# Performance work log

Measured on AMD Instinct MI355X. Metric: run time of the kernel, lower is better.

Reference implementation:

```python
import jax, jax.numpy as jnp
import numpy as np

# ---- static config ----
SCALES = [1, 2, 3, 4, 6, 9, 13, 19, 27, 40, 60, 88, 128]
L = sum(SCALES)            # 400
FIRST_L = SCALES[0]        # 1
C = 1024                   # emb_dim (C == D)
DEPTH = 8
H = 16
DH = C // H
CVAE = 64
V = 4096
ND = 256                   # node_embed_size
MLP = 4 * C
B = 32
EPS = 1e-6

_LVL = np.concatenate([np.full(pn, i, dtype=np.int32) for i, pn in enumerate(SCALES)])  # [L]
_BIAS = np.where(_LVL[:, None] >= _LVL[None, :], 0.0, -np.inf).astype(np.float32)        # [L,L]


def _ln(x):
    # LayerNorm without affine params (VAR's ln_wo_grad), eps=1e-6
    m = jnp.mean(x, axis=-1, keepdims=True)
    v = jnp.mean(jnp.square(x - m), axis=-1, keepdims=True)
    return (x - m) * jax.lax.rsqrt(v + EPS)


def setup_inputs() -> dict:
    key = jax.random.key(0)
    ks = iter(jax.random.split(key, 40))
    def p(shape, s=0.02):
        return jax.random.normal(next(ks), shape, dtype=jnp.float32) * s
    inp = {
        "x_BLCv_wo_first_l": jax.random.normal(next(ks), (B, L - FIRST_L, CVAE), jnp.float32),
        "poc_context": jax.random.normal(next(ks), (B, L, CVAE), jnp.float32),
        "poc_cond": jax.random.normal(next(ks), (B, ND), jnp.float32),
        # embedders / positional
        "word_w": p((CVAE, C)), "word_b": p((C,)),
        "poc_w": p((ND, C)), "poc_b": p((C,)),
        "pos_start": p((1, FIRST_L, C)),
        "pos_1LC": p((1, L, C)),
        "lvl_tab": p((len(SCALES), C)),
        # shared AdaLN (SiLU -> Linear(D, 6C))
        "ada_w": p((C, 6 * C)), "ada_b": p((6 * C,)),
        # per-block params, stacked over depth
        "ada_gss": p((DEPTH, 1, 1, 6, C)),
        "q_w": p((DEPTH, C, C)), "q_b": p((DEPTH, C)),
        "kv_w": p((DEPTH, C, 2 * C)), "kv_b": p((DEPTH, 2 * C)),
        "proj_w": p((DEPTH, C, C)), "proj_b": p((DEPTH, C)),
        "fc1_w": p((DEPTH, C, MLP)), "fc1_b": p((DEPTH, MLP)),
        "fc2_w": p((DEPTH, MLP, C)), "fc2_b": p((DEPTH, C)),
        # AdaLNBeforeHead (SiLU -> Linear(D, 2C)) + head
        "head_ada_w": p((C, 2 * C)), "head_ada_b": p((2 * C,)),
        "head_w": p((C, V)), "head_b": p((V,)),
    }
    return inp


def reference(x_BLCv_wo_first_l, poc_context, poc_cond,
              word_w, word_b, poc_w, poc_b, pos_start, pos_1LC, lvl_tab,
              ada_w, ada_b, ada_gss, q_w, q_b, kv_w, kv_b, proj_w, proj_b,
              fc1_w, fc1_b, fc2_w, fc2_b, head_ada_w, head_ada_b, head_w, head_b):
    lvl_idx = jnp.asarray(_LVL)
    bias = jnp.asarray(_BIAS)                      # [L,L] block scale-causal
    scale = 1.0 / np.sqrt(DH)

    cond = poc_cond @ poc_w + poc_b                # [B,C] (cond_BD == sos source)
    sos = cond[:, None, :] + pos_start             # [B,first_l,C]
    x = jnp.concatenate([sos, x_BLCv_wo_first_l @ word_w + word_b], axis=1)  # [B,L,C]
    lvl = lvl_tab[lvl_idx] + pos_1LC[0]            # [L,C]
    x = x + lvl
    poc = (poc_context @ word_w + word_b) + lvl    # [B,L,C]

    gss = jax.nn.silu(cond) @ ada_w + ada_b        # [B,6C]
    gss = gss.reshape(B, 1, 6, C)

    def block(x, params):
        ag, qw, qb, kvw, kvb, pw, pb, f1w, f1b, f2w, f2b = params
        mod = ag + gss                             # [B,1,6,C]
        g1, g2, s1, s2, sh1, sh2 = [mod[:, :, i] for i in range(6)]  # each [B,1,C]
        # cross-attention (q from modulated x, kv from poc context), scale-causal bias
        xn = _ln(x) * (1.0 + s1) + sh1
        q = (xn @ qw + qb).reshape(B, L, H, DH)
        kv = (poc @ kvw + kvb).reshape(B, L, 2, H, DH)
        k, v = kv[:, :, 0], kv[:, :, 1]
        att = jnp.einsum('bqhd,bkhd->bhqk', q, k) * scale + bias
        att = jax.nn.softmax(att, axis=-1)
        o = jnp.einsum('bhqk,bkhd->bqhd', att, v).reshape(B, L, C)
        x = x + g1 * (o @ pw + pb)
        # FFN with AdaLN modulation
        xn2 = _ln(x) * (1.0 + s2) + sh2
        hdn = jax.nn.gelu(xn2 @ f1w + f1b, approximate=False)
        x = x + g2 * (hdn @ f2w + f2b)
        return x, None

    x, _ = jax.lax.scan(block, x, (ada_gss, q_w, q_b, kv_w, kv_b, proj_w, proj_b,
                                   fc1_w, fc1_b, fc2_w, fc2_b))

    # AdaLNBeforeHead + head
    ss = jax.nn.silu(cond) @ head_ada_w + head_ada_b   # [B,2C]
    h_scale, h_shift = ss[:, None, :C], ss[:, None, C:]
    x = _ln(x) * (1.0 + h_scale) + h_shift
    logits = x @ head_w + head_b                       # [B,L,V]
    return logits
```

## Files before the change

kernel.cpp:

```cpp
#include <hip/hip_runtime.h>
#include <hip/hip_bf16.h>
#include <math.h>

#define DEV __device__ __forceinline__

typedef __attribute__((ext_vector_type(4))) float f32x4;
typedef __attribute__((ext_vector_type(8))) short bf16x8;
typedef __attribute__((ext_vector_type(4))) short s16x4;

static constexpr int Bz = 32, Lz = 400, Cz = 1024, MLPz = 4096;
static constexpr int BL = Bz * Lz;

DEV float bf2f(unsigned short u) {
  union { unsigned int i; float f; } v; v.i = ((unsigned int)u) << 16; return v.f;
}
DEV unsigned short f2bf(float f) {
  union { float f; unsigned int i; } v; v.f = f;
  unsigned int r = v.i + 0x7FFFu + ((v.i >> 16) & 1u);
  return (unsigned short)(r >> 16);
}

DEV int level_of(int l) {
  const int cum[13] = {1,3,6,10,16,25,38,57,84,124,184,272,400};
  int lv = 12;
  #pragma unroll
  for (int i = 12; i >= 0; i--) if (l < cum[i]) lv = i;
  return lv;
}
DEV int row_kmax(int l) {
  const int cum[13] = {1,3,6,10,16,25,38,57,84,124,184,272,400};
  int km = 400;
  #pragma unroll
  for (int i = 12; i >= 0; i--) if (l < cum[i]) km = cum[i];
  return km;
}

DEV void stage16(const unsigned short* g, unsigned short* l) {
#if __has_builtin(__builtin_amdgcn_global_load_lds)
  __builtin_amdgcn_global_load_lds((const __attribute__((address_space(1))) void*)g,
                                   (__attribute__((address_space(3))) void*)l, 16, 0, 0);
#else
  *(bf16x8*)l = *(const bf16x8*)g;
#endif
}

__global__ __launch_bounds__(256)
void tconv_k(const float* __restrict__ in, unsigned short* __restrict__ out, int K, int N)
{
  __shared__ float t[64][65];
  const int n0 = blockIdx.x * 64, k0 = blockIdx.y * 64;
  #pragma unroll
  for (int i = 0; i < 16; i++) {
    int idx = i * 256 + threadIdx.x;
    int r = idx >> 6, c = idx & 63;
    t[r][c] = in[(size_t)(k0 + r) * N + n0 + c];
  }
  __syncthreads();
  #pragma unroll
  for (int i = 0; i < 16; i++) {
    int idx = i * 256 + threadIdx.x;
    int rn = idx >> 6, ck = idx & 63;
    out[(size_t)(n0 + rn) * K + k0 + ck] = f2bf(t[ck][rn]);
  }
}

__global__ __launch_bounds__(256)
void tconv5_k(const float* __restrict__ qw, const float* __restrict__ kvw,
              const float* __restrict__ pjw, const float* __restrict__ f1w,
              unsigned short* __restrict__ qwt, unsigned short* __restrict__ kvwt,
              unsigned short* __restrict__ pjwt, unsigned short* __restrict__ f1wt)
{
  const int bid = blockIdx.x;
  const float* in; unsigned short* out; int N, n0, k0;
  if (bid < 256)       { in = qw;  out = qwt;  N = 1024; int t = bid;        n0 = (t & 15) * 64; k0 = (t >> 4) * 64; }
  else if (bid < 768)  { in = kvw; out = kvwt; N = 2048; int t = bid - 256;  n0 = (t & 31) * 64; k0 = (t >> 5) * 64; }
  else if (bid < 1024) { in = pjw; out = pjwt; N = 1024; int t = bid - 768;  n0 = (t & 15) * 64; k0 = (t >> 4) * 64; }
  else                 { in = f1w; out = f1wt; N = 4096; int t = bid - 1024; n0 = (t & 63) * 64; k0 = (t >> 6) * 64; }
  __shared__ float tt[64][65];
  #pragma unroll
  for (int i = 0; i < 16; i++) {
    int idx = i * 256 + threadIdx.x;
    int r = idx >> 6, c = idx & 63;
    tt[r][c] = in[(size_t)(k0 + r) * N + n0 + c];
  }
  __syncthreads();
  #pragma unroll
  for (int i = 0; i < 16; i++) {
    int idx = i * 256 + threadIdx.x;
    int rn = idx >> 6, ck = idx & 63;
    out[(size_t)(n0 + rn) * 1024 + k0 + ck] = f2bf(tt[ck][rn]);
  }
}

enum { EP_BF16 = 0, EP_GELU = 1, EP_RESID = 2, EP_F32 = 3, EP_KV = 4 };

template<int MODE>
__global__ __launch_bounds__(256, 2)
void gemm2_k(const unsigned short* __restrict__ A, const unsigned short* __restrict__ Bt,
             const float* __restrict__ bias, void* __restrict__ out,
             float* __restrict__ xres, const float* __restrict__ gsh,
             const float* __restrict__ gpb, unsigned short* __restrict__ vtb,
             int N, int K)
{
  __shared__ unsigned short As[128 * 64];
  __shared__ unsigned short Bs[128 * 64];
  const int tid = threadIdx.x;
  const int lane = tid & 63, wv = tid >> 6;
  const int row0 = blockIdx.x * 128, col0 = blockIdx.y * 128;
  const int wm = (wv >> 1) * 64, wn = (wv & 1) * 64;

  f32x4 acc[4][4] = {};

  for (int k0 = 0; k0 < K; k0 += 64) {
    #pragma unroll
    for (int i = 0; i < 4; i++) {
      int ch = i * 256 + tid;
      int r = ch >> 3;
      int c8 = (ch & 7) ^ (r & 7);
      stage16(A + (size_t)(row0 + r) * K + k0 + c8 * 8, As + ch * 8);
    }
    #pragma unroll
    for (int i = 0; i < 4; i++) {
      int ch = i * 256 + tid;
      int r = ch >> 3;
      int c8 = (ch & 7) ^ (r & 7);
      stage16(Bt + (size_t)(col0 + r) * K + k0 + c8 * 8, Bs + ch * 8);
    }
    __syncthreads();
    #pragma unroll
    for (int kk = 0; kk < 2; kk++) {
      bf16x8 af[4], bfr[4];
      const int bcol = kk * 64 + (lane >> 4) * 16;
      #pragma unroll
      for (int m = 0; m < 4; m++) {
        int r = wm + m * 16 + (lane & 15);
        af[m] = *(const bf16x8*)((char*)As + r * 128 + (bcol ^ ((r & 7) << 4)));
      }
      #pragma unroll
      for (int n = 0; n < 4; n++) {
        int r = wn + n * 16 + (lane & 15);
        bfr[n] = *(const bf16x8*)((char*)Bs + r * 128 + (bcol ^ ((r & 7) << 4)));
      }
      #pragma unroll
      for (int m = 0; m < 4; m++)
        #pragma unroll
        for (int n = 0; n < 4; n++)
          acc[m][n] = __builtin_amdgcn_mfma_f32_16x16x32_bf16(af[m], bfr[n], acc[m][n], 0, 0, 0);
    }
    __syncthreads();
  }

  const int rbase = row0 + wm + ((lane >> 4) << 2);
  const int cbase = col0 + wn + (lane & 15);
  #pragma unroll
  for (int n = 0; n < 4; n++) {
    int gcol = cbase + n * 16;
    float bv = bias[gcol];
    #pragma unroll
    for (int m = 0; m < 4; m++) {
      #pragma unroll
      for (int r = 0; r < 4; r++) {
        int grow = rbase + m * 16 + r;
        float v = acc[m][n][r] + bv;
        if constexpr (MODE == EP_BF16) {
          ((unsigned short*)out)[(size_t)grow * N + gcol] = f2bf(v);
        } else if constexpr (MODE == EP_GELU) {
          float g = 0.5f * v * (1.f + erff(v * 0.70710678118654752f));
          ((unsigned short*)out)[(size_t)grow * N + gcol] = f2bf(g);
        } else if constexpr (MODE == EP_RESID) {
          int b = grow / Lz;
          float g = gsh[gcol] + gpb[(size_t)b * 6144 + gcol];
          xres[(size_t)grow * Cz + gcol] += g * v;
        } else if constexpr (MODE == EP_KV) {
          if (gcol < 1024) {
            ((unsigned short*)out)[(size_t)grow * 1024 + gcol] = f2bf(v);
          } else {
            int b = grow / Lz, l = grow - b * Lz;
            int h = (gcol >> 6) & 15, d = gcol & 63;
            vtb[(((size_t)b * 16 + h) * 64 + d) * Lz + l] = f2bf(v);
          }
        } else {
          ((float*)out)[(size_t)grow * N + gcol] = v;
        }
      }
    }
  }
}

__global__ __launch_bounds__(256, 2)
void qkv_k(const unsigned short* __restrict__ xn, const unsigned short* __restrict__ poc,
           const unsigned short* __restrict__ qwt, const unsigned short* __restrict__ kvwt,
           const float* __restrict__ q_bias, const float* __restrict__ kv_bias,
           unsigned short* __restrict__ qbf, unsigned short* __restrict__ kbuf,
           unsigned short* __restrict__ vtb)
{
  __shared__ unsigned short As[128 * 64];
  __shared__ unsigned short Bs[128 * 64];
  const int tid = threadIdx.x;
  const int lane = tid & 63, wv = tid >> 6;
  const bool isq = blockIdx.y < 8;
  const unsigned short* A  = isq ? xn : poc;
  const unsigned short* Bt = isq ? qwt : kvwt;
  const float* bias        = isq ? q_bias : kv_bias;
  const int K = 1024;
  const int row0 = blockIdx.x * 128;
  const int col0 = (isq ? blockIdx.y : (blockIdx.y - 8)) * 128;
  const int wm = (wv >> 1) * 64, wn = (wv & 1) * 64;

  f32x4 acc[4][4] = {};

  for (int k0 = 0; k0 < K; k0 += 64) {
    #pragma unroll
    for (int i = 0; i < 4; i++) {
      int ch = i * 256 + tid;
      int r = ch >> 3;
      int c8 = (ch & 7) ^ (r & 7);
      stage16(A + (size_t)(row0 + r) * K + k0 + c8 * 8, As + ch * 8);
    }
    #pragma unroll
    for (int i = 0; i < 4; i++) {
      int ch = i * 256 + tid;
      int r = ch >> 3;
      int c8 = (ch & 7) ^ (r & 7);
      stage16(Bt + (size_t)(col0 + r) * K + k0 + c8 * 8, Bs + ch * 8);
    }
    __syncthreads();
    #pragma unroll
    for (int kk = 0; kk < 2; kk++) {
      bf16x8 af[4], bfr[4];
      const int bcol = kk * 64 + (lane >> 4) * 16;
      #pragma unroll
      for (int m = 0; m < 4; m++) {
        int r = wm + m * 16 + (lane & 15);
        af[m] = *(const bf16x8*)((char*)As + r * 128 + (bcol ^ ((r & 7) << 4)));
      }
      #pragma unroll
      for (int n = 0; n < 4; n++) {
        int r = wn + n * 16 + (lane & 15);
        bfr[n] = *(const bf16x8*)((char*)Bs + r * 128 + (bcol ^ ((r & 7) << 4)));
      }
      #pragma unroll
      for (int m = 0; m < 4; m++)
        #pragma unroll
        for (int n = 0; n < 4; n++)
          acc[m][n] = __builtin_amdgcn_mfma_f32_16x16x32_bf16(af[m], bfr[n], acc[m][n], 0, 0, 0);
    }
    __syncthreads();
  }

  const int rbase = row0 + wm + ((lane >> 4) << 2);
  const int cbase = col0 + wn + (lane & 15);
  #pragma unroll
  for (int n = 0; n < 4; n++) {
    int gcol = cbase + n * 16;
    float bv = bias[gcol];
    #pragma unroll
    for (int m = 0; m < 4; m++) {
      #pragma unroll
      for (int r = 0; r < 4; r++) {
        int grow = rbase + m * 16 + r;
        float v = acc[m][n][r] + bv;
        if (isq) {
          qbf[(size_t)grow * 1024 + gcol] = f2bf(v);
        } else if (gcol < 1024) {
          kbuf[(size_t)grow * 1024 + gcol] = f2bf(v);
        } else {
          int b = grow / Lz, l = grow - b * Lz;
          int h = (gcol >> 6) & 15, d = gcol & 63;
          vtb[(((size_t)b * 16 + h) * 64 + d) * Lz + l] = f2bf(v);
        }
      }
    }
  }
}

__global__ __launch_bounds__(256)
void ln2_k(const float* __restrict__ x, unsigned short* __restrict__ out,
           const float* __restrict__ ssh, const float* __restrict__ spb, int sstride,
           const float* __restrict__ hsh, const float* __restrict__ hpb, int hstride)
{
  const int wv = threadIdx.x >> 6, lane = threadIdx.x & 63;
  const int row = blockIdx.x * 4 + wv;
  const int b = row / Lz;
  const float* xr = x + (size_t)row * Cz;
  f32x4 v[4];
  float s1 = 0.f;
  #pragma unroll
  for (int j = 0; j < 4; j++) {
    v[j] = *(const f32x4*)(xr + j * 256 + lane * 4);
    s1 += v[j][0] + v[j][1] + v[j][2] + v[j][3];
  }
  #pragma unroll
  for (int o = 32; o > 0; o >>= 1) s1 += __shfl_xor(s1, o, 64);
  float mean = s1 * (1.f / 1024.f);
  float s2 = 0.f;
  #pragma unroll
  for (int j = 0; j < 4; j++)
    #pragma unroll
    for (int i = 0; i < 4; i++) { float d = v[j][i] - mean; s2 += d * d; }
  #pragma unroll
  for (int o = 32; o > 0; o >>= 1) s2 += __shfl_xor(s2, o, 64);
  float rstd = rsqrtf(s2 * (1.f / 1024.f) + 1e-6f);
  #pragma unroll
  for (int j = 0; j < 4; j++) {
    s16x4 o4;
    #pragma unroll
    for (int i = 0; i < 4; i++) {
      int c = j * 256 + lane * 4 + i;
      float sc = (ssh ? ssh[c] : 0.f) + spb[(size_t)b * sstride + c];
      float sh = (hsh ? hsh[c] : 0.f) + hpb[(size_t)b * hstride + c];
      o4[i] = (short)f2bf((v[j][i] - mean) * rstd * (1.f + sc) + sh);
    }
    *(s16x4*)(&out[(size_t)row * Cz + j * 256 + lane * 4]) = o4;
  }
}

__global__ __launch_bounds__(512)
void attn3_k(const unsigned short* __restrict__ qb,
             const unsigned short* __restrict__ kbuf,
             const unsigned short* __restrict__ vtb,
             unsigned short* __restrict__ ob)
{
  __shared__ unsigned short Ks[400 * 64];
  __shared__ unsigned short Vt[64 * 408];
  __shared__ unsigned short Pl[8][512];
  const int bh = blockIdx.x, b = bh >> 4, h = bh & 15;
  const int qc = blockIdx.y;
  const int tid = threadIdx.x;
  const int q0 = qc * 128;
  const int nch = (row_kmax(min(q0 + 127, Lz - 1)) + 15) >> 4;

  const size_t kbase = (size_t)b * Lz * 1024 + h * 64;
  for (int i = tid; i < nch * 128; i += 512) {
    int l = i >> 3, d8 = i & 7;
    bf16x8 kr = *(const bf16x8*)&kbuf[kbase + (size_t)l * 1024 + d8 * 8];
    *(bf16x8*)((char*)Ks + l * 128 + ((d8 * 16) ^ ((l & 7) << 4))) = kr;
  }
  const size_t vbase = ((size_t)b * 16 + h) * 64 * Lz;
  const int vch = nch * 2;
  for (int i = tid; i < 3200; i += 512) {
    int d = i / 50, c8 = i - d * 50;
    if (c8 < vch)
      *(bf16x8*)((char*)Vt + d * 816 + c8 * 16) = *(const bf16x8*)&vtb[vbase + (size_t)d * Lz + c8 * 8];
  }
  __syncthreads();

  const int wv = tid >> 6, lane = tid & 63, g = lane >> 4, q = lane & 15;
  const int qw0 = q0 + wv * 16;
  if (qw0 >= Lz) return;
  const int qrow = qw0 + q;
  const int my_kmax = row_kmax(qrow);
  const int nsch = (row_kmax(qw0 + 15) + 31) >> 5;
  const int vclamp = nch * 16 - 8;

  const unsigned short* qp = qb + (size_t)(b * Lz + qrow) * Cz + h * 64;
  bf16x8 qf0 = *(const bf16x8*)(qp + g * 8);
  bf16x8 qf1 = *(const bf16x8*)(qp + 32 + g * 8);
  unsigned short* myP = &Pl[wv][0];

  float m = -30000.f, lsum = 0.f;
  f32x4 acc[4] = {};

  for (int sc = 0; sc < nsch; ++sc) {
    f32x4 st0 = {0.f,0.f,0.f,0.f}, st1 = {0.f,0.f,0.f,0.f};
    {
      int kr = sc * 32 + q;
      const char* kb = (const char*)Ks + kr * 128;
      int sw = (kr & 7) << 4;
      bf16x8 k0 = *(const bf16x8*)(kb + ((g * 16) ^ sw));
      bf16x8 k1 = *(const bf16x8*)(kb + ((64 + g * 16) ^ sw));
      st0 = __builtin_amdgcn_mfma_f32_16x16x32_bf16(k0, qf0, st0, 0, 0, 0);
      st0 = __builtin_amdgcn_mfma_f32_16x16x32_bf16(k1, qf1, st0, 0, 0, 0);
    }
    {
      int kr = sc * 32 + 16 + q;
      const char* kb = (const char*)Ks + kr * 128;
      int sw = (kr & 7) << 4;
      bf16x8 k0 = *(const bf16x8*)(kb + ((g * 16) ^ sw));
      bf16x8 k1 = *(const bf16x8*)(kb + ((64 + g * 16) ^ sw));
      st1 = __builtin_amdgcn_mfma_f32_16x16x32_bf16(k0, qf0, st1, 0, 0, 0);
      st1 = __builtin_amdgcn_mfma_f32_16x16x32_bf16(k1, qf1, st1, 0, 0, 0);
    }

    float s8[8]; float cmax = -30000.f;
    #pragma unroll
    for (int r = 0; r < 4; r++) {
      int k0g = sc * 32 + 4 * g + r;
      int k1g = k0g + 16;
      s8[r]     = (k0g < my_kmax) ? st0[r] * 0.125f : -30000.f;
      s8[4 + r] = (k1g < my_kmax) ? st1[r] * 0.125f : -30000.f;
      cmax = fmaxf(cmax, fmaxf(s8[r], s8[4 + r]));
    }
    cmax = fmaxf(cmax, __shfl_xor(cmax, 16, 64));
    cmax = fmaxf(cmax, __shfl_xor(cmax, 32, 64));

    if (!__all(cmax <= m + 8.f)) {
      float mnew = fmaxf(m, cmax);
      float f = __expf(m - mnew);
      lsum *= f;
      #pragma unroll
      for (int blk = 0; blk < 4; blk++)
        #pragma unroll
        for (int j = 0; j < 4; j++) acc[blk][j] *= f;
      m = mnew;
    }

    float p[8], ps = 0.f;
    #pragma unroll
    for (int r = 0; r < 8; r++) { p[r] = __expf(s8[r] - m); ps += p[r]; }
    ps += __shfl_xor(ps, 16, 64);
    ps += __shfl_xor(ps, 32, 64);
    lsum += ps;

    #pragma unroll
    for (int cp = 0; cp < 2; cp++) {
      #pragma unroll
      for (int j = 0; j < 2; j++) {
        unsigned int pk;
        asm("v_cvt_pk_bf16_f32 %0, %1, %2" : "=v"(pk)
            : "v"(p[4 * cp + 2 * j]), "v"(p[4 * cp + 2 * j + 1]));
        int w = 8 * cp + 2 * g + j;
        *(unsigned int*)((char*)myP + q * 64 + 4 * (w ^ q)) = pk;
      }
    }

    unsigned int pw[4];
    #pragma unroll
    for (int i = 0; i < 4; i++)
      pw[i] = *(const unsigned int*)((const char*)myP + q * 64 + 4 * ((4 * g + i) ^ q));
    bf16x8 pfrag;
    #pragma unroll
    for (int i = 0; i < 4; i++) {
      pfrag[2 * i]     = (short)(pw[i] & 0xFFFF);
      pfrag[2 * i + 1] = (short)(pw[i] >> 16);
    }

    const int koff = min(sc * 32 + 8 * g, vclamp);
    #pragma unroll
    for (int blk = 0; blk < 4; blk++) {
      bf16x8 vf = *(const bf16x8*)((const char*)Vt + (16 * blk + q) * 816 + koff * 2);
      acc[blk] = __builtin_amdgcn_mfma_f32_16x16x32_bf16(vf, pfrag, acc[blk], 0, 0, 0);
    }
  }

  float inv = 1.f / lsum;
  unsigned short* op = ob + (size_t)(b * Lz + qrow) * Cz + h * 64;
  #pragma unroll
  for (int blk = 0; blk < 4; blk++)
    #pragma unroll
    for (int r = 0; r < 4; r++)
      op[16 * blk + 4 * g + r] = f2bf(acc[blk][r] * inv);
}

__global__ __launch_bounds__(256)
void cond_k(const float* __restrict__ pc, const float* __restrict__ pw,
            const float* __restrict__ pb, float* __restrict__ cond,
            float* __restrict__ silu)
{
  const int b = blockIdx.y;
  const int n = blockIdx.x * 256 + threadIdx.x;
  __shared__ float a[256];
  a[threadIdx.x] = pc[b * 256 + threadIdx.x];
  __syncthreads();
  float s = pb[n];
  for (int k = 0; k < 256; k++) s += a[k] * pw[(size_t)k * Cz + n];
  cond[(size_t)b * Cz + n] = s;
  silu[(size_t)b * Cz + n] = s / (1.f + __expf(-s));
}

__global__ __launch_bounds__(256)
void smallmm_k(const float* __restrict__ A, const float* __restrict__ W,
               const float* __restrict__ bias, float* __restrict__ out, int N)
{
  const int b = blockIdx.y;
  const int n = blockIdx.x * 256 + threadIdx.x;
  __shared__ float a[1024];
  for (int i = threadIdx.x; i < 1024; i += 256) a[i] = A[(size_t)b * 1024 + i];
  __syncthreads();
  float s = bias[n];
  for (int k = 0; k < 1024; k++) s += a[k] * W[(size_t)k * N + n];
  out[(size_t)b * N + n] = s;
}

__global__ __launch_bounds__(256)
void embed2_k(const float* __restrict__ src0, const float* __restrict__ src1,
              const float* __restrict__ ww, const float* __restrict__ wb,
              const float* __restrict__ cond, const float* __restrict__ pos_start,
              const float* __restrict__ pos1, const float* __restrict__ ltab,
              float* __restrict__ out0, unsigned short* __restrict__ out1)
{
  const int MODE = blockIdx.y;
  const int r0 = blockIdx.x * 4;
  const int tid = threadIdx.x;
  const int b = r0 / Lz;
  __shared__ float a[4][64];
  {
    int rr = tid >> 6, k = tid & 63;
    int l = (r0 + rr) % Lz;
    float val;
    if (MODE == 0) val = (l == 0) ? 0.f : src0[((size_t)b * (Lz - 1) + (l - 1)) * 64 + k];
    else           val = src1[((size_t)(r0 + rr)) * 64 + k];
    a[rr][k] = val;
  }
  __syncthreads();
  #pragma unroll
  for (int ci = 0; ci < 4; ci++) {
    int c = tid + ci * 256;
    float s[4];
    #pragma unroll
    for (int rr = 0; rr < 4; rr++) {
      int l = (r0 + rr) % Lz;
      s[rr] = wb[c] + ltab[(size_t)level_of(l) * Cz + c] + pos1[(size_t)l * Cz + c];
    }
    for (int k = 0; k < 64; k++) {
      float w = ww[(size_t)k * Cz + c];
      #pragma unroll
      for (int rr = 0; rr < 4; rr++) s[rr] += a[rr][k] * w;
    }
    #pragma unroll
    for (int rr = 0; rr < 4; rr++) {
      int l = (r0 + rr) % Lz;
      if (MODE == 0) {
        float val = s[rr];
        if (l == 0) val = cond[(size_t)b * Cz + c] + pos_start[c] + ltab[c] + pos1[c];
        out0[((size_t)(r0 + rr)) * Cz + c] = val;
      } else {
        out1[((size_t)(r0 + rr)) * Cz + c] = f2bf(s[rr]);
      }
    }
  }
}

extern "C" void kernel_launch(void* const* d_in, const int* in_sizes, int n_in,
                              void* d_out, int out_size, void* d_ws, size_t ws_size,
                              hipStream_t stream)
{
  (void)in_sizes; (void)n_in; (void)out_size; (void)ws_size;
  const float* x_blcv   = (const float*)d_in[0];
  const float* poc_ctx  = (const float*)d_in[1];
  const float* poc_cond = (const float*)d_in[2];
  const float* word_w   = (const float*)d_in[3];
  const float* word_b   = (const float*)d_in[4];
  const float* poc_w    = (const float*)d_in[5];
  const float* poc_b    = (const float*)d_in[6];
  const float* pos_start= (const float*)d_in[7];
  const float* pos_1lc  = (const float*)d_in[8];
  const float* lvl_tab  = (const float*)d_in[9];
  const float* ada_w    = (const float*)d_in[10];
  const float* ada_b    = (const float*)d_in[11];
  const float* ada_gss  = (const float*)d_in[12];
  const float* q_w      = (const float*)d_in[13];
  const float* q_b      = (const float*)d_in[14];
  const float* kv_w     = (const float*)d_in[15];
  const float* kv_b     = (const float*)d_in[16];
  const float* proj_w   = (const float*)d_in[17];
  const float* proj_b   = (const float*)d_in[18];
  const float* fc1_w    = (const float*)d_in[19];
  const float* fc1_b    = (const float*)d_in[20];
  const float* fc2_w    = (const float*)d_in[21];
  const float* fc2_b    = (const float*)d_in[22];
  const float* head_ada_w = (const float*)d_in[23];
  const float* head_ada_b = (const float*)d_in[24];
  const float* head_w   = (const float*)d_in[25];
  const float* head_b   = (const float*)d_in[26];

  char* p = (char*)d_ws;
  auto carve = [&](size_t bytes) { void* r = (void*)p; p += (bytes + 255) & ~(size_t)255; return r; };
  float* x            = (float*)carve((size_t)BL * Cz * 4);
  unsigned short* xn  = (unsigned short*)carve((size_t)BL * Cz * 2);
  unsigned short* poc = (unsigned short*)carve((size_t)BL * Cz * 2);
  unsigned short* qbf = (unsigned short*)carve((size_t)BL * Cz * 2);
  unsigned short* kbuf= (unsigned short*)carve((size_t)BL * Cz * 2);
  unsigned short* vtb = (unsigned short*)carve((size_t)BL * Cz * 2);
  unsigned short* ob  = (unsigned short*)carve((size_t)BL * Cz * 2);
  unsigned short* hdn = (unsigned short*)carve((size_t)BL * MLPz * 2);
  unsigned short* wt  = (unsigned short*)carve((size_t)12582912 * 2);
  float* cond  = (float*)carve(32 * 1024 * 4);
  float* siluc = (float*)carve(32 * 1024 * 4);
  float* gss   = (float*)carve(32 * 6144 * 4);
  float* ss    = (float*)carve(32 * 2048 * 4);

  unsigned short* qwt  = wt;
  unsigned short* kvwt = wt + 1048576;
  unsigned short* pjwt = wt + 3145728;
  unsigned short* f1wt = wt + 4194304;
  unsigned short* f2wt = wt + 8388608;

  cond_k<<<dim3(4, 32), 256, 0, stream>>>(poc_cond, poc_w, poc_b, cond, siluc);
  smallmm_k<<<dim3(24, 32), 256, 0, stream>>>(siluc, ada_w, ada_b, gss, 6144);
  smallmm_k<<<dim3(8, 32), 256, 0, stream>>>(siluc, head_ada_w, head_ada_b, ss, 2048);
  embed2_k<<<dim3(3200, 2), 256, 0, stream>>>(x_blcv, poc_ctx, word_w, word_b, cond,
                                              pos_start, pos_1lc, lvl_tab, x, poc);

  for (int d = 0; d < 8; d++) {
    const float* ag = ada_gss + (size_t)d * 6144;
    tconv5_k<<<2048, 256, 0, stream>>>(
        q_w + (size_t)d * 1048576, kv_w + (size_t)d * 2097152,
        proj_w + (size_t)d * 1048576, fc1_w + (size_t)d * 4194304,
        qwt, kvwt, pjwt, f1wt);
    tconv_k<<<dim3(16, 64), 256, 0, stream>>>(fc2_w + (size_t)d * 4194304, f2wt, 4096, 1024);

    ln2_k<<<3200, 256, 0, stream>>>(x, xn, ag + 2 * 1024, gss + 2 * 1024, 6144,
                                    ag + 4 * 1024, gss + 4 * 1024, 6144);
    qkv_k<<<dim3(100, 24), 256, 0, stream>>>(
        xn, poc, qwt, kvwt, q_b + d * 1024, kv_b + d * 2048, qbf, kbuf, vtb);
    attn3_k<<<dim3(512, 4), 512, 0, stream>>>(qbf, kbuf, vtb, ob);
    gemm2_k<EP_RESID><<<dim3(100, 8), 256, 0, stream>>>(
        ob, pjwt, proj_b + d * 1024, nullptr, x, ag + 0, gss + 0, nullptr, 1024, 1024);
    ln2_k<<<3200, 256, 0, stream>>>(x, xn, ag + 3 * 1024, gss + 3 * 1024, 6144,
                                    ag + 5 * 1024, gss + 5 * 1024, 6144);
    gemm2_k<EP_GELU><<<dim3(100, 32), 256, 0, stream>>>(
        xn, f1wt, fc1_b + d * 4096, hdn, nullptr, nullptr, nullptr, nullptr, 4096, 1024);
    gemm2_k<EP_RESID><<<dim3(100, 8), 256, 0, stream>>>(
        hdn, f2wt, fc2_b + d * 1024, nullptr, x, ag + 1024, gss + 1024, nullptr, 1024, 4096);
  }
  ln2_k<<<3200, 256, 0, stream>>>(x, xn, nullptr, ss, 2048, nullptr, ss + 1024, 2048);
  tconv_k<<<dim3(64, 16), 256, 0, stream>>>(head_w, wt, 1024, 4096);
  gemm2_k<EP_F32><<<dim3(100, 32), 256, 0, stream>>>(
      xn, wt, head_b, d_out, nullptr, nullptr, nullptr, nullptr, 4096, 1024);
}
```

Baseline: 6.105 ms.

## Run input embedding GEMMs on MFMA with bf16-converted inputs

Replaces the scalar fp32 embedding kernel with three steps: convert the word and poc-context inputs to bf16, transpose the word weights, then run a 128x128 tiled MFMA GEMM with K=64. Bias, level and positional adds and the first-token special case are applied in the GEMM epilogue. This targets the scalar FMA cost of the embedding step, at the price of bf16 rounding on the residual-stream input x and two extra small launches.

```diff
diff --git a/kernel.cpp b/kernel.cpp
--- a/kernel.cpp
+++ b/kernel.cpp
@@ -275,6 +275,112 @@
 }
 
 __global__ __launch_bounds__(256)
+void eprep_k(const float* __restrict__ src0, const float* __restrict__ src1,
+             unsigned short* __restrict__ A0, unsigned short* __restrict__ A1)
+{
+  const int chunk = blockIdx.x * 256 + threadIdx.x;
+  const int row = chunk >> 3, k8 = (chunk & 7) * 8;
+  bf16x8 o;
+  if (blockIdx.y == 0) {
+    const int b = row / Lz, l = row - b * Lz;
+    if (l == 0) {
+      #pragma unroll
+      for (int i = 0; i < 8; i++) o[i] = 0;
+    } else {
+      const float* s = src0 + ((size_t)b * (Lz - 1) + (l - 1)) * 64 + k8;
+      #pragma unroll
+      for (int i = 0; i < 8; i++) o[i] = (short)f2bf(s[i]);
+    }
+    *(bf16x8*)(A0 + (size_t)row * 64 + k8) = o;
+  } else {
+    const float* s = src1 + (size_t)row * 64 + k8;
+    #pragma unroll
+    for (int i = 0; i < 8; i++) o[i] = (short)f2bf(s[i]);
+    *(bf16x8*)(A1 + (size_t)row * 64 + k8) = o;
+  }
+}
+
+__global__ __launch_bounds__(256, 2)
+void egemm_k(const unsigned short* __restrict__ A0, const unsigned short* __restrict__ A1,
+             const unsigned short* __restrict__ wwt, const float* __restrict__ wb,
+             const float* __restrict__ ltab, const float* __restrict__ pos1,
+             const float* __restrict__ cond, const float* __restrict__ pos_start,
+             float* __restrict__ xout, unsigned short* __restrict__ pocout)
+{
+  __shared__ unsigned short As[128 * 64];
+  __shared__ unsigned short Bs[128 * 64];
+  const int tid = threadIdx.x;
+  const int lane = tid & 63, wv = tid >> 6;
+  const int mode = blockIdx.y >> 3;
+  const int col0 = (blockIdx.y & 7) * 128;
+  const int row0 = blockIdx.x * 128;
+  const unsigned short* A = mode ? A1 : A0;
+  const int wm = (wv >> 1) * 64, wn = (wv & 1) * 64;
+
+  f32x4 acc[4][4] = {};
+
+  #pragma unroll
+  for (int i = 0; i < 4; i++) {
+    int ch = i * 256 + tid;
+    int r = ch >> 3;
+    int c8 = (ch & 7) ^ (r & 7);
+    stage16(A + (size_t)(row0 + r) * 64 + c8 * 8, As + ch * 8);
+  }
+  #pragma unroll
+  for (int i = 0; i < 4; i++) {
+    int ch = i * 256 + tid;
+    int r = ch >> 3;
+    int c8 = (ch & 7) ^ (r & 7);
+    stage16(wwt + (size_t)(col0 + r) * 64 + c8 * 8, Bs + ch * 8);
+  }
+  __syncthreads();
+  #pragma unroll
+  for (int kk = 0; kk < 2; kk++) {
+    bf16x8 af[4], bfr[4];
+    const int bcol = kk * 64 + (lane >> 4) * 16;
+    #pragma unroll
+    for (int m = 0; m < 4; m++) {
+      int r = wm + m * 16 + (lane & 15);
+      af[m] = *(const bf16x8*)((char*)As + r * 128 + (bcol ^ ((r & 7) << 4)));
+    }
+    #pragma unroll
+    for (int n = 0; n < 4; n++) {
+      int r = wn + n * 16 + (lane & 15);
+      bfr[n] = *(const bf16x8*)((char*)Bs + r * 128 + (bcol ^ ((r & 7) << 4)));
+    }
+    #pragma unroll
+    for (int m = 0; m < 4; m++)
+      #pragma unroll
+      for (int n = 0; n < 4; n++)
+        acc[m][n] = __builtin_amdgcn_mfma_f32_16x16x32_bf16(af[m], bfr[n], acc[m][n], 0, 0, 0);
+  }
+
+  const int rbase = row0 + wm + ((lane >> 4) << 2);
+  const int cbase = col0 + wn + (lane & 15);
+  #pragma unroll
+  for (int n = 0; n < 4; n++) {
+    int gcol = cbase + n * 16;
+    float bv = wb[gcol];
+    #pragma unroll
+    for (int m = 0; m < 4; m++) {
+      #pragma unroll
+      for (int r = 0; r < 4; r++) {
+        int grow = rbase + m * 16 + r;
+        int b = grow / Lz, l = grow - b * Lz;
+        float base = ltab[(size_t)level_of(l) * Cz + gcol] + pos1[(size_t)l * Cz + gcol];
+        float v = acc[m][n][r] + bv + base;
+        if (mode == 0) {
+          if (l == 0) v = cond[(size_t)b * Cz + gcol] + pos_start[gcol] + ltab[gcol] + pos1[gcol];
+          xout[(size_t)grow * Cz + gcol] = v;
+        } else {
+          pocout[(size_t)grow * Cz + gcol] = f2bf(v);
+        }
+      }
+    }
+  }
+}
+
+__global__ __launch_bounds__(256)
 void ln2_k(const float* __restrict__ x, unsigned short* __restrict__ out,
            const float* __restrict__ ssh, const float* __restrict__ spb, int sstride,
            const float* __restrict__ hsh, const float* __restrict__ hpb, int hstride)
@@ -480,55 +586,6 @@
   float s = bias[n];
   for (int k = 0; k < 1024; k++) s += a[k] * W[(size_t)k * N + n];
   out[(size_t)b * N + n] = s;
-}
-
-__global__ __launch_bounds__(256)
-void embed2_k(const float* __restrict__ src0, const float* __restrict__ src1,
-              const float* __restrict__ ww, const float* __restrict__ wb,
-              const float* __restrict__ cond, const float* __restrict__ pos_start,
-              const float* __restrict__ pos1, const float* __restrict__ ltab,
-              float* __restrict__ out0, unsigned short* __restrict__ out1)
-{
-  const int MODE = blockIdx.y;
-  const int r0 = blockIdx.x * 4;
-  const int tid = threadIdx.x;
-  const int b = r0 / Lz;
-  __shared__ float a[4][64];
-  {
-    int rr = tid >> 6, k = tid & 63;
-    int l = (r0 + rr) % Lz;
-    float val;
-    if (MODE == 0) val = (l == 0) ? 0.f : src0[((size_t)b * (Lz - 1) + (l - 1)) * 64 + k];
-    else           val = src1[((size_t)(r0 + rr)) * 64 + k];
-    a[rr][k] = val;
-  }
-  __syncthreads();
-  #pragma unroll
-  for (int ci = 0; ci < 4; ci++) {
-    int c = tid + ci * 256;
-    float s[4];
-    #pragma unroll
-    for (int rr = 0; rr < 4; rr++) {
-      int l = (r0 + rr) % Lz;
-      s[rr] = wb[c] + ltab[(size_t)level_of(l) * Cz + c] + pos1[(size_t)l * Cz + c];
-    }
-    for (int k = 0; k < 64; k++) {
-      float w = ww[(size_t)k * Cz + c];
-      #pragma unroll
-      for (int rr = 0; rr < 4; rr++) s[rr] += a[rr][k] * w;
-    }
-    #pragma unroll
-    for (int rr = 0; rr < 4; rr++) {
-      int l = (r0 + rr) % Lz;
-      if (MODE == 0) {
-        float val = s[rr];
-        if (l == 0) val = cond[(size_t)b * Cz + c] + pos_start[c] + ltab[c] + pos1[c];
-        out0[((size_t)(r0 + rr)) * Cz + c] = val;
-      } else {
-        out1[((size_t)(r0 + rr)) * Cz + c] = f2bf(s[rr]);
-      }
-    }
-  }
 }
 
 extern "C" void kernel_launch(void* const* d_in, const int* in_sizes, int n_in,
@@ -575,6 +632,9 @@
   unsigned short* ob  = (unsigned short*)carve((size_t)BL * Cz * 2);
   unsigned short* hdn = (unsigned short*)carve((size_t)BL * MLPz * 2);
   unsigned short* wt  = (unsigned short*)carve((size_t)12582912 * 2);
+  unsigned short* A0  = (unsigned short*)carve((size_t)BL * 64 * 2);
+  unsigned short* A1  = (unsigned short*)carve((size_t)BL * 64 * 2);
+  unsigned short* wwt = (unsigned short*)carve((size_t)1024 * 64 * 2);
   float* cond  = (float*)carve(32 * 1024 * 4);
   float* siluc = (float*)carve(32 * 1024 * 4);
   float* gss   = (float*)carve(32 * 6144 * 4);
@@ -589,8 +649,10 @@
   cond_k<<<dim3(4, 32), 256, 0, stream>>>(poc_cond, poc_w, poc_b, cond, siluc);
   smallmm_k<<<dim3(24, 32), 256, 0, stream>>>(siluc, ada_w, ada_b, gss, 6144);
   smallmm_k<<<dim3(8, 32), 256, 0, stream>>>(siluc, head_ada_w, head_ada_b, ss, 2048);
-  embed2_k<<<dim3(3200, 2), 256, 0, stream>>>(x_blcv, poc_ctx, word_w, word_b, cond,
-                                              pos_start, pos_1lc, lvl_tab, x, poc);
+  eprep_k<<<dim3(400, 2), 256, 0, stream>>>(x_blcv, poc_ctx, A0, A1);
+  tconv_k<<<dim3(16, 1), 256, 0, stream>>>(word_w, wwt, 64, 1024);
+  egemm_k<<<dim3(100, 16), 256, 0, stream>>>(A0, A1, wwt, word_b, lvl_tab, pos_1lc,
+                                             cond, pos_start, x, poc);
 
   for (int d = 0; d < 8; d++) {
     const float* ag = ada_gss + (size_t)d * 6144;
```

New measurement: 5.939 ms (median of 2 runs). 2.7% less time.
